# Kernel tuning notes

Measured on AMD Instinct MI355X. Metric: run time of the kernel, lower is better.

Reference implementation:

```python
import jax, jax.numpy as jnp
import numpy as np
from functools import partial

B, S, T = 32, 64, 64
VS, VT = 32000, 32000
E, H = 256, 512            # embed_dim, encoder hidden per direction
DH = 2 * H                 # decoder hidden (= encoder_hidden_dim)
A = 128                    # attention_dim


def _p(key, shape, scale=0.05):
    return scale * jax.random.normal(key, shape, dtype=jnp.float32)


def setup_inputs() -> dict:
    key = jax.random.key(0)
    ks = jax.random.split(key, 32)
    inp = {
        'src': jax.random.randint(ks[0], (B, S), 0, VS),
        'tgt_input': jax.random.randint(ks[1], (B, T), 0, VT),
        # encoder
        'enc_emb': _p(ks[2], (VS, E)),
        'enc_Wih_f': _p(ks[3], (4 * H, E)), 'enc_Whh_f': _p(ks[4], (4 * H, H)),
        'enc_bih_f': _p(ks[5], (4 * H,)),  'enc_bhh_f': _p(ks[6], (4 * H,)),
        'enc_Wih_b': _p(ks[7], (4 * H, E)), 'enc_Whh_b': _p(ks[8], (4 * H, H)),
        'enc_bih_b': _p(ks[9], (4 * H,)),  'enc_bhh_b': _p(ks[10], (4 * H,)),
        # decoder
        'dec_emb': _p(ks[11], (VT, E)),
        'Wd': _p(ks[12], (A, DH)), 'bd': _p(ks[13], (A,)),
        'We': _p(ks[14], (A, DH)), 'be': _p(ks[15], (A,)),
        'v_att': _p(ks[16], (A,)), 'bv': _p(ks[17], ()),
        'dec_Wih': _p(ks[18], (4 * DH, E + DH)), 'dec_Whh': _p(ks[19], (4 * DH, DH)),
        'dec_bih': _p(ks[20], (4 * DH,)), 'dec_bhh': _p(ks[21], (4 * DH,)),
        'Wo': _p(ks[22], (VT, DH + DH)), 'bo': _p(ks[23], (VT,)),
    }
    return inp


def _lstm_cell(x, h, c, Wih, Whh, b):
    g = x @ Wih.T + h @ Whh.T + b
    i, f, gg, o = jnp.split(g, 4, axis=-1)  # PyTorch gate order: i,f,g,o
    i, f, o = jax.nn.sigmoid(i), jax.nn.sigmoid(f), jax.nn.sigmoid(o)
    c_new = f * c + i * jnp.tanh(gg)
    h_new = o * jnp.tanh(c_new)
    return h_new, c_new


def _lstm_scan(xs, Wih, Whh, b, reverse):
    # xs: [S,B,E] -> outputs [S,B,H] aligned with input positions, final (h,c)
    h0 = jnp.zeros((xs.shape[1], Whh.shape[1]), xs.dtype)
    def step(carry, x):
        h, c = carry
        h, c = _lstm_cell(x, h, c, Wih, Whh, b)
        return (h, c), h
    (hT, cT), hs = jax.lax.scan(step, (h0, h0), xs, reverse=reverse)
    return hs, hT, cT


def _forward(src, tgt_input, enc_emb,
             enc_Wih_f, enc_Whh_f, enc_bih_f, enc_bhh_f,
             enc_Wih_b, enc_Whh_b, enc_bih_b, enc_bhh_b,
             dec_emb, Wd, bd, We, be, v_att, bv,
             dec_Wih, dec_Whh, dec_bih, dec_bhh, Wo, bo):
    # ---- Encoder: bidirectional single-layer LSTM ----
    emb = enc_emb[src]                              # [B,S,E]
    xs = emb.transpose(1, 0, 2)                     # [S,B,E]
    hs_f, hT_f, cT_f = _lstm_scan(xs, enc_Wih_f, enc_Whh_f, enc_bih_f + enc_bhh_f, False)
    hs_b, hT_b, cT_b = _lstm_scan(xs, enc_Wih_b, enc_Whh_b, enc_bih_b + enc_bhh_b, True)
    enc_out = jnp.concatenate([hs_f, hs_b], axis=-1).transpose(1, 0, 2)  # [B,S,2H]
    h = jnp.concatenate([hT_f, hT_b], axis=-1)      # [B,DH]
    c = jnp.concatenate([cT_f, cT_b], axis=-1)

    # ---- Decoder with Bahdanau attention (full teacher forcing) ----
    enc_proj = enc_out @ We.T + be                  # [B,S,A] precomputed
    dec_b = dec_bih + dec_bhh
    tgt_emb = dec_emb[tgt_input].transpose(1, 0, 2)  # [T,B,E]

    def dec_step(carry, emb_t):
        h, c = carry
        dproj = h @ Wd.T + bd                       # [B,A]
        energy = jnp.tanh(dproj[:, None, :] + enc_proj)  # [B,S,A]
        scores = energy @ v_att + bv                # [B,S]
        w = jax.nn.softmax(scores, axis=1)
        ctx = jnp.einsum('bs,bsh->bh', w, enc_out)  # [B,DH]
        x = jnp.concatenate([emb_t, ctx], axis=-1)  # [B,E+DH]
        h_new, c_new = _lstm_cell(x, h, c, dec_Wih, dec_Whh, dec_b)
        logits = jnp.concatenate([h_new, ctx], axis=-1) @ Wo.T + bo  # [B,VT]
        return (h_new, c_new), logits

    _, logits = jax.lax.scan(dec_step, (h, c), tgt_emb)  # [T,B,VT]
    return logits.transpose(1, 0, 2)                     # [B,T,VT]


def reference(src, tgt_input, enc_emb,
              enc_Wih_f, enc_Whh_f, enc_bih_f, enc_bhh_f,
              enc_Wih_b, enc_Whh_b, enc_bih_b, enc_bhh_b,
              dec_emb, Wd, bd, We, be, v_att, bv,
              dec_Wih, dec_Whh, dec_bih, dec_bhh, Wo, bo):
    return _forward(src, tgt_input, enc_emb,
                    enc_Wih_f, enc_Whh_f, enc_bih_f, enc_bhh_f,
                    enc_Wih_b, enc_Whh_b, enc_bih_b, enc_bhh_b,
                    dec_emb, Wd, bd, We, be, v_att, bv,
                    dec_Wih, dec_Whh, dec_bih, dec_bhh, Wo, bo)
```

## Files before the change

kernel.cpp:

```cpp
#include <hip/hip_runtime.h>


using u16 = unsigned short;
using u32 = unsigned int;
using u64 = unsigned long long;
using f32x4 = __attribute__((ext_vector_type(4))) float;
using s16x8 = __attribute__((ext_vector_type(8))) short;
using u16x4 = __attribute__((ext_vector_type(4))) unsigned short;

__device__ __forceinline__ float sigm_(float x) { return 1.0f / (1.0f + expf(-x)); }
__device__ __forceinline__ float tanh_(float x) {
    float e = __expf(fminf(2.0f * x, 30.0f));
    return (e - 1.0f) / (e + 1.0f);
}

__device__ __forceinline__ u16 f2bf(float x) {
    u32 u = __float_as_uint(x);
    u += 0x7fffu + ((u >> 16) & 1u);
    return (u16)(u >> 16);
}
__device__ __forceinline__ u32 pk2(float a, float b) {
    return (u32)f2bf(a) | ((u32)f2bf(b) << 16);
}
__device__ __forceinline__ float bf2f(u16 v) {
    return __uint_as_float((u32)v << 16);
}

__device__ __forceinline__ void ast32(u32* p, u32 v) {
    __hip_atomic_store(p, v, __ATOMIC_RELAXED, __HIP_MEMORY_SCOPE_AGENT);
}

#define MFMA __builtin_amdgcn_mfma_f32_16x16x32_bf16

#define GLL(g, l) __builtin_amdgcn_global_load_lds( \
    (__attribute__((address_space(1))) void*)(g),   \
    (__attribute__((address_space(3))) void*)(l), 16, 0, 0)

__device__ __forceinline__ void poll8(const int* go8) {
    if (threadIdx.x < 8) {
        const int* p = go8 + threadIdx.x * 16;
        while (__hip_atomic_load(p, __ATOMIC_RELAXED, __HIP_MEMORY_SCOPE_AGENT) == 0)
            __builtin_amdgcn_s_sleep(1);
    }
    __syncthreads();
    asm volatile("" ::: "memory");
}
__device__ __forceinline__ void arrive8(int* cnt8, int* go8, int line, int perline) {
    asm volatile("s_waitcnt vmcnt(0) lgkmcnt(0)" ::: "memory");
    __syncthreads();
    if (threadIdx.x == 0) {
        int old = __hip_atomic_fetch_add(cnt8 + line * 16, 1, __ATOMIC_RELAXED,
                                         __HIP_MEMORY_SCOPE_AGENT);
        if (old == perline - 1)
            __hip_atomic_store(go8 + line * 16, 1, __ATOMIC_RELAXED, __HIP_MEMORY_SCOPE_AGENT);
    }
}

__global__ __launch_bounds__(256) void k_zero(float* __restrict__ p, int n) {
    int i = blockIdx.x * 256 + threadIdx.x;
    if (i < n) p[i] = 0.0f;
}

__global__ __launch_bounds__(256) void k_cast_bf16(const float* __restrict__ in,
                                                   u16* __restrict__ outp, int n8) {
    int idx = blockIdx.x * 256 + threadIdx.x;
    if (idx >= n8) return;
    const f32x4* p = (const f32x4*)in + (size_t)idx * 2;
    f32x4 a = p[0], c = p[1];
    u32* o = (u32*)(outp + (size_t)idx * 8);
    o[0] = pk2(a.x, a.y); o[1] = pk2(a.z, a.w);
    o[2] = pk2(c.x, c.y); o[3] = pk2(c.z, c.w);
}

__global__ __launch_bounds__(256) void k_embed_bf(const int* __restrict__ tok,
                                                  const float* __restrict__ emb,
                                                  u16* __restrict__ outp) {
    int idx = blockIdx.x * 256 + threadIdx.x;
    int r = idx >> 6, e4 = idx & 63;
    int outer = r >> 5, b = r & 31;
    int tk = tok[b * 64 + outer];
    f32x4 v = ((const f32x4*)emb)[(size_t)tk * 64 + e4];
    u32* o = (u32*)(outp + (size_t)r * 256 + (e4 << 2));
    o[0] = pk2(v.x, v.y); o[1] = pk2(v.z, v.w);
}

__global__ __launch_bounds__(256) void k_prep_perm(
    const float* __restrict__ src, u16* __restrict__ dst,
    int J, int K4, int srcStride, int srcOff, int total)
{
    int idx = blockIdx.x * 256 + threadIdx.x;
    if (idx >= total) return;
    int n = idx / K4, kq = (idx - n * K4) << 2;
    int orig = (n & 3) * J + (n >> 2);
    f32x4 v = *(const f32x4*)(src + (size_t)orig * srcStride + srcOff + kq);
    u32* o = (u32*)(dst + (size_t)n * (K4 << 2) + kq);
    o[0] = pk2(v.x, v.y); o[1] = pk2(v.z, v.w);
}

__global__ __launch_bounds__(256) void k_prep_ws(
    const float* __restrict__ W, u16* __restrict__ dst)
{
    int idx = blockIdx.x * 256 + threadIdx.x;
    int n = idx >> 8, kp = idx & 255, k0 = kp << 1;
    int orig = (n & 3) * 512 + (n >> 2);
    const float* s = W + (size_t)orig * 512 + k0;
    int g = n >> 5, r = n & 31;
    int byteoff = (k0 << 1) ^ ((r & 7) << 4);
    *(u32*)((char*)dst + (size_t)g * 32768 + r * 1024 + byteoff) = pk2(s[0], s[1]);
}

__global__ __launch_bounds__(256) void k_prep_w2s(
    const float* __restrict__ Whh, const float* __restrict__ Wih, u16* __restrict__ dst)
{
    int idx = blockIdx.x * 256 + threadIdx.x;
    int n = idx >> 10, kp = idx & 1023, k0 = kp << 1;
    int orig = (n & 3) * 1024 + (n >> 2);
    const float* s = (k0 < 1024) ? (Whh + (size_t)orig * 1024 + k0)
                                 : (Wih + (size_t)orig * 1280 + 256 + (k0 - 1024));
    int g = n >> 5, r = n & 31;
    int byteoff = (k0 << 1) ^ ((r & 7) << 4);
    *(u32*)((char*)dst + (size_t)g * 131072 + r * 4096 + byteoff) = pk2(s[0], s[1]);
}

__global__ __launch_bounds__(256) void k_gemm_bf(
    const u16* __restrict__ A, const u16* __restrict__ B, int K,
    const float* __restrict__ b1, const float* __restrict__ b2, int biasJ,
    float* __restrict__ C, int ldc, int nM, int nN, int remapOut, int swz)
{
    __shared__ __align__(16) u16 As[128 * 32];
    __shared__ __align__(16) u16 Bs[128 * 32];
    int w = blockIdx.x;
    if (swz) { int cpx = (nM * nN) >> 3; w = (w & 7) * cpx + (w >> 3); }
    int bm = (w % nM) * 128, bn = (w / nM) * 128;
    int tid = threadIdx.x, wave = tid >> 6, lane = tid & 63;
    int wm = wave & 1, wn = wave >> 1;
    f32x4 acc[4][4] = {};

    int rA = wave * 32 + (lane >> 2);
    int cb2 = (lane & 3) * 16;
    const char* gA = (const char*)A + ((size_t)(bm + rA) * K) * 2 + cb2;
    const char* gB = (const char*)B + ((size_t)(bn + rA) * K) * 2 + cb2;
    size_t rowskip = (size_t)16 * K * 2;
    char* lA = (char*)As + wave * 2048;
    char* lB = (char*)Bs + wave * 2048;
    const u16* rdA = As + (wm * 64 + (lane & 15)) * 32 + (lane >> 4) * 8;
    const u16* rdB = Bs + (wn * 64 + (lane & 15)) * 32 + (lane >> 4) * 8;

    for (int k0 = 0; k0 < K; k0 += 32) {
        size_t kb = (size_t)k0 * 2;
        GLL(gA + kb, lA); GLL(gA + kb + rowskip, lA + 1024);
        GLL(gB + kb, lB); GLL(gB + kb + rowskip, lB + 1024);
        __syncthreads();
        s16x8 af[4], bfv[4];
#pragma unroll
        for (int m2 = 0; m2 < 4; ++m2) af[m2] = *(const s16x8*)(rdA + m2 * 512);
#pragma unroll
        for (int n2 = 0; n2 < 4; ++n2) bfv[n2] = *(const s16x8*)(rdB + n2 * 512);
#pragma unroll
        for (int m2 = 0; m2 < 4; ++m2)
#pragma unroll
            for (int n2 = 0; n2 < 4; ++n2)
                acc[m2][n2] = MFMA(af[m2], bfv[n2], acc[m2][n2], 0, 0, 0);
        __syncthreads();
    }

    int rbase = bm + wm * 64 + ((lane >> 4) << 2);
    int cbase = bn + wn * 64 + (lane & 15);
#pragma unroll
    for (int n2 = 0; n2 < 4; ++n2) {
        int col = cbase + n2 * 16;
        int bcol = biasJ ? ((col & 3) * biasJ + (col >> 2)) : col;
        float bias = (b1 ? b1[bcol] : 0.0f) + (b2 ? b2[bcol] : 0.0f);
#pragma unroll
        for (int m2 = 0; m2 < 4; ++m2) {
            f32x4 v = acc[m2][n2];
#pragma unroll
            for (int jj = 0; jj < 4; ++jj) {
                int row = rbase + m2 * 16 + jj;
                int orow = remapOut ? ((row & 31) * 64 + (row >> 5)) : row;
                C[(size_t)orow * ldc + col] = v[jj] + bias;
            }
        }
    }
}

__global__ __launch_bounds__(256, 1) void k_enc_persist(
    const u16* __restrict__ Wsf, const u16* __restrict__ Wsb,
    const float* __restrict__ Gfp, const float* __restrict__ Gbp,
    u16* __restrict__ henc,
    float* __restrict__ cfb,
    u16* __restrict__ encbf,
    int* __restrict__ cnt8, int* __restrict__ go8)
{
    __shared__ __align__(16) char smem[50176];
    int tid = threadIdx.x, lane = tid & 63, q = tid >> 6;
    int dir = blockIdx.x >> 6, g = blockIdx.x & 63;
    const char* wsrc = (const char*)(dir ? Wsb : Wsf) + (size_t)g * 32768;
#pragma unroll
    for (int it = 0; it < 8; ++it)
        GLL(wsrc + it * 4096 + tid * 16, smem + it * 4096 + tid * 16);
    __syncthreads();

    float* sacc = (float*)(smem + 32768);
    u16* hst = (u16*)(smem + 49664);
    const float* Gp = dir ? Gbp : Gfp;
    float* cB = cfb + dir * 16384;
    int lr = lane & 15, lk = (lane >> 4) << 3;
    int bb = tid & 31, jl = tid >> 5;
    int n0 = g * 32, j = g * 8 + jl;

    for (int s = 0; s < 64; ++s) {
        if (s) poll8(go8 + s * 128);
        int t = dir ? (63 - s) : s;
        f32x4 p4 = *(const f32x4*)(Gp + ((size_t)(t * 32 + bb)) * 2048 + n0 + (jl << 2));
        const u16* hA = henc + (size_t)s * 32768 + dir * 16384;
        s16x8 afr[8];
#pragma unroll
        for (int it = 0; it < 4; ++it) {
            int ke = q * 128 + it * 32 + lk;
            afr[2 * it]     = *(const s16x8*)(hA + lr * 512 + ke);
            afr[2 * it + 1] = *(const s16x8*)(hA + (lr + 16) * 512 + ke);
        }
        f32x4 acc00 = {}, acc01 = {}, acc10 = {}, acc11 = {};
#pragma unroll
        for (int it = 0; it < 4; ++it) {
            int ke = q * 128 + it * 32 + lk;
            int kb = ke << 1;
            s16x8 b0 = *(const s16x8*)(smem + lr * 1024 + (kb ^ ((lr & 7) << 4)));
            int r1 = lr + 16;
            s16x8 b1 = *(const s16x8*)(smem + r1 * 1024 + (kb ^ ((r1 & 7) << 4)));
            acc00 = MFMA(afr[2 * it], b0, acc00, 0, 0, 0);
            acc01 = MFMA(afr[2 * it], b1, acc01, 0, 0, 0);
            acc10 = MFMA(afr[2 * it + 1], b0, acc10, 0, 0, 0);
            acc11 = MFMA(afr[2 * it + 1], b1, acc11, 0, 0, 0);
        }
        int rw = (lane >> 4) << 2;
#pragma unroll
        for (int rr = 0; rr < 4; ++rr) {
            sacc[q * 1056 + (rw + rr) * 33 + lr]        = acc00[rr];
            sacc[q * 1056 + (rw + rr) * 33 + 16 + lr]   = acc01[rr];
            sacc[q * 1056 + (16 + rw + rr) * 33 + lr]      = acc10[rr];
            sacc[q * 1056 + (16 + rw + rr) * 33 + 16 + lr] = acc11[rr];
        }
        __syncthreads();
        {
            int c4 = jl << 2;
            float gi = 0, gf = 0, gg = 0, go2 = 0;
#pragma unroll
            for (int q2 = 0; q2 < 4; ++q2) {
                const float* sp = sacc + q2 * 1056 + bb * 33 + c4;
                gi += sp[0]; gf += sp[1]; gg += sp[2]; go2 += sp[3];
            }
            gi += p4.x; gf += p4.y; gg += p4.z; go2 += p4.w;
            float* cp = cB + bb * 512 + j;
            float cn = sigm_(gf) * cp[0] + sigm_(gi) * tanhf(gg);
            cp[0] = cn;
            float h = sigm_(go2) * tanhf(cn);
            u16 h16 = f2bf(h);
            encbf[((size_t)(bb * 64 + t)) * 1024 + dir * 512 + j] = h16;
            hst[bb * 8 + jl] = h16;
        }
        __syncthreads();
        if (tid < 128) {
            int bb2 = tid >> 2, p2 = tid & 3;
            u32 wv = (u32)hst[bb2 * 8 + 2 * p2] | ((u32)hst[bb2 * 8 + 2 * p2 + 1] << 16);
            ast32((u32*)(henc + (size_t)(s + 1) * 32768 + dir * 16384) + bb2 * 256 + g * 4 + p2, wv);
        }
        arrive8(cnt8 + (s + 1) * 128, go8 + (s + 1) * 128, blockIdx.x & 7, 16);
    }
}

__global__ __launch_bounds__(256) void k_dec_init(
    const u16* __restrict__ henc, const float* __restrict__ cfb,
    u16* __restrict__ hcarr, float* __restrict__ cd)
{
    int idx = blockIdx.x * 256 + threadIdx.x;
    int b = idx >> 10, j = idx & 1023;
    int dir = (j >> 9), jj = j & 511;
    hcarr[b * 2048 + j] = henc[(size_t)64 * 32768 + dir * 16384 + b * 512 + jj];
    cd[b * 1024 + j] = cfb[dir * 16384 + b * 512 + jj];
}

__global__ __launch_bounds__(256, 1) void k_dec_persist(
    const u16* __restrict__ W2s, const u16* __restrict__ encbf,
    const float* __restrict__ Prep,
    const u16* __restrict__ Wd_bf, const float* __restrict__ bd,
    const float* __restrict__ eproj, const float* __restrict__ v_att,
    const float* __restrict__ bv,
    u16* __restrict__ hcarr, float* __restrict__ cd, u16* __restrict__ Abf,
    int* __restrict__ hCnt8, int* __restrict__ goH8,
    int* __restrict__ ctxCnt8, int* __restrict__ goCtx8)
{
    __shared__ __align__(16) char smem[148480];
    int blk = blockIdx.x, tid = threadIdx.x, lane = tid & 63, q = tid >> 6;
    bool isgate = blk < 128;
    {
        const char* src = isgate ? ((const char*)W2s + (size_t)blk * 131072)
                                 : ((const char*)encbf + (size_t)(blk - 128) * 131072);
#pragma unroll
        for (int it = 0; it < 32; ++it)
            GLL(src + it * 4096 + tid * 16, smem + it * 4096 + tid * 16);
    }
    __syncthreads();

    float* sacc = (float*)(smem + 131072);
    u16* hst    = (u16*)(smem + 147968);
    float* hsh  = (float*)(smem + 131072);
    float* red  = (float*)(smem + 135168);
    float* dp   = (float*)(smem + 136192);
    float* sc   = (float*)(smem + 136704);

    int lr = lane & 15, lk = (lane >> 4) << 3;
    int bb = tid & 31, jl = tid >> 5;
    int n0 = blk * 32, j = blk * 8 + jl;
    int b = blk - 128;

    for (int t = 0; t < 64; ++t) {
        if (t) poll8(goH8 + t * 128);
        const u16* hcT = hcarr + (size_t)t * 65536;
        if (isgate) {
            f32x4 p4 = *(const f32x4*)(Prep + ((size_t)(t * 32 + bb)) * 4096 + n0 + (jl << 2));
            s16x8 afr[16];
#pragma unroll
            for (int it = 0; it < 8; ++it) {
                int ke = q * 256 + it * 32 + lk;
                afr[2 * it]     = *(const s16x8*)(hcT + lr * 2048 + ke);
                afr[2 * it + 1] = *(const s16x8*)(hcT + (lr + 16) * 2048 + ke);
            }
            f32x4 acc00 = {}, acc01 = {}, acc10 = {}, acc11 = {};
#pragma unroll
            for (int it = 0; it < 8; ++it) {
                int ke = q * 256 + it * 32 + lk;
                int kb = ke << 1;
                s16x8 b0 = *(const s16x8*)(smem + lr * 4096 + (kb ^ ((lr & 7) << 4)));
                int r1 = lr + 16;
                s16x8 b1 = *(const s16x8*)(smem + r1 * 4096 + (kb ^ ((r1 & 7) << 4)));
                acc00 = MFMA(afr[2 * it], b0, acc00, 0, 0, 0);
                acc01 = MFMA(afr[2 * it], b1, acc01, 0, 0, 0);
                acc10 = MFMA(afr[2 * it + 1], b0, acc10, 0, 0, 0);
                acc11 = MFMA(afr[2 * it + 1], b1, acc11, 0, 0, 0);
            }
            poll8(goCtx8 + t * 128);
#pragma unroll
            for (int it = 0; it < 8; ++it) {
                int ke = 1024 + q * 256 + it * 32 + lk;
                afr[2 * it]     = *(const s16x8*)(hcT + lr * 2048 + ke);
                afr[2 * it + 1] = *(const s16x8*)(hcT + (lr + 16) * 2048 + ke);
            }
#pragma unroll
            for (int it = 0; it < 8; ++it) {
                int ke = 1024 + q * 256 + it * 32 + lk;
                int kb = ke << 1;
                s16x8 b0 = *(const s16x8*)(smem + lr * 4096 + (kb ^ ((lr & 7) << 4)));
                int r1 = lr + 16;
                s16x8 b1 = *(const s16x8*)(smem + r1 * 4096 + (kb ^ ((r1 & 7) << 4)));
                acc00 = MFMA(afr[2 * it], b0, acc00, 0, 0, 0);
                acc01 = MFMA(afr[2 * it], b1, acc01, 0, 0, 0);
                acc10 = MFMA(afr[2 * it + 1], b0, acc10, 0, 0, 0);
                acc11 = MFMA(afr[2 * it + 1], b1, acc11, 0, 0, 0);
            }
            int rw = (lane >> 4) << 2;
#pragma unroll
            for (int rr = 0; rr < 4; ++rr) {
                sacc[q * 1056 + (rw + rr) * 33 + lr]        = acc00[rr];
                sacc[q * 1056 + (rw + rr) * 33 + 16 + lr]   = acc01[rr];
                sacc[q * 1056 + (16 + rw + rr) * 33 + lr]      = acc10[rr];
                sacc[q * 1056 + (16 + rw + rr) * 33 + 16 + lr] = acc11[rr];
            }
            __syncthreads();
            {
                int c4 = jl << 2;
                float gi = 0, gf = 0, gg = 0, go2 = 0;
#pragma unroll
                for (int q2 = 0; q2 < 4; ++q2) {
                    const float* sp = sacc + q2 * 1056 + bb * 33 + c4;
                    gi += sp[0]; gf += sp[1]; gg += sp[2]; go2 += sp[3];
                }
                gi += p4.x; gf += p4.y; gg += p4.z; go2 += p4.w;
                int ci = bb * 1024 + j;
                float cn = sigm_(gf) * cd[ci] + sigm_(gi) * tanhf(gg);
                cd[ci] = cn;
                float h = sigm_(go2) * tanhf(cn);
                u16 h16 = f2bf(h);
                Abf[((size_t)(t * 32 + bb)) * 2048 + j] = h16;
                hst[bb * 8 + jl] = h16;
            }
            __syncthreads();
            if (tid < 128) {
                int bb2 = tid >> 2, p2 = tid & 3;
                u32 wv = (u32)hst[bb2 * 8 + 2 * p2] | ((u32)hst[bb2 * 8 + 2 * p2 + 1] << 16);
                ast32((u32*)(hcarr + (size_t)(t + 1) * 65536) + bb2 * 1024 + blk * 4 + p2, wv);
            }
            arrive8(hCnt8 + (t + 1) * 128, goH8 + (t + 1) * 128, blk & 7, 16);
        } else {
            {
                u16x4 hv = *(const u16x4*)(hcT + b * 2048 + (tid << 2));
                hsh[(tid << 2) + 0] = bf2f(hv.x);
                hsh[(tid << 2) + 1] = bf2f(hv.y);
                hsh[(tid << 2) + 2] = bf2f(hv.z);
                hsh[(tid << 2) + 3] = bf2f(hv.w);
            }
            __syncthreads();
            {
                int a = tid & 127, half = tid >> 7;
                const u16* wr = Wd_bf + ((size_t)a << 10) + (half << 9);
                const float* hh = hsh + (half << 9);
                float s0 = 0, s1 = 0, s2 = 0, s3 = 0;
#pragma unroll 4
                for (int k = 0; k < 512; k += 32) {
                    s16x8 w0 = *(const s16x8*)(wr + k);
                    s16x8 w1 = *(const s16x8*)(wr + k + 8);
                    s16x8 w2 = *(const s16x8*)(wr + k + 16);
                    s16x8 w3 = *(const s16x8*)(wr + k + 24);
#pragma unroll
                    for (int e = 0; e < 8; ++e) {
                        s0 += bf2f((u16)w0[e]) * hh[k + e];
                        s1 += bf2f((u16)w1[e]) * hh[k + 8 + e];
                        s2 += bf2f((u16)w2[e]) * hh[k + 16 + e];
                        s3 += bf2f((u16)w3[e]) * hh[k + 24 + e];
                    }
                }
                red[tid] = (s0 + s1) + (s2 + s3);
            }
            __syncthreads();
            if (tid < 128) dp[tid] = red[tid] + red[tid + 128] + bd[tid];
            __syncthreads();
            {
                int si = tid >> 2, qq = tid & 3;
                const float* ep = eproj + ((size_t)(b * 64 + si)) * 128 + qq * 32;
                float s = 0.0f;
#pragma unroll 8
                for (int a2 = 0; a2 < 32; ++a2)
                    s += v_att[qq * 32 + a2] * tanh_(dp[qq * 32 + a2] + ep[a2]);
                red[tid] = s;
            }
            __syncthreads();
            if (tid < 64) {
                float x = red[tid * 4] + red[tid * 4 + 1] + red[tid * 4 + 2] + red[tid * 4 + 3] + bv[0];
                float mx = x;
#pragma unroll
                for (int off = 32; off; off >>= 1) mx = fmaxf(mx, __shfl_xor(mx, off));
                float e = __expf(x - mx), ss = e;
#pragma unroll
                for (int off = 32; off; off >>= 1) ss += __shfl_xor(ss, off);
                sc[tid] = e / ss;
            }
            __syncthreads();
            u32 cw0, cw1;
            {
                const u16* eL = (const u16*)smem;
                int c0i = tid << 2;
                float c0 = 0, c1 = 0, c2 = 0, c3 = 0;
                for (int s2 = 0; s2 < 64; ++s2) {
                    float wgt = sc[s2];
                    u16x4 rp = *(const u16x4*)(eL + s2 * 1024 + c0i);
                    c0 += wgt * bf2f(rp.x); c1 += wgt * bf2f(rp.y);
                    c2 += wgt * bf2f(rp.z); c3 += wgt * bf2f(rp.w);
                }
                cw0 = pk2(c0, c1); cw1 = pk2(c2, c3);
                u32* hw = (u32*)hcT + b * 1024 + 512 + (tid << 1);
                ast32(hw, cw0); ast32(hw + 1, cw1);
            }
            arrive8(ctxCnt8 + t * 128, goCtx8 + t * 128, blk & 7, 4);
            {
                u32* aw = (u32*)(Abf + ((size_t)(t * 32 + b)) * 2048 + 1024 + (tid << 2));
                aw[0] = cw0; aw[1] = cw1;
            }
        }
    }
}

extern "C" void kernel_launch(void* const* d_in, const int* in_sizes, int n_in,
                              void* d_out, int out_size, void* d_ws, size_t ws_size,
                              hipStream_t stream)
{
    (void)in_sizes; (void)n_in; (void)out_size; (void)ws_size;
    const int*   src     = (const int*)d_in[0];
    const int*   tgt     = (const int*)d_in[1];
    const float* enc_emb = (const float*)d_in[2];
    const float* eWih_f  = (const float*)d_in[3];
    const float* eWhh_f  = (const float*)d_in[4];
    const float* ebih_f  = (const float*)d_in[5];
    const float* ebhh_f  = (const float*)d_in[6];
    const float* eWih_b  = (const float*)d_in[7];
    const float* eWhh_b  = (const float*)d_in[8];
    const float* ebih_b  = (const float*)d_in[9];
    const float* ebhh_b  = (const float*)d_in[10];
    const float* dec_emb = (const float*)d_in[11];
    const float* Wd      = (const float*)d_in[12];
    const float* bd      = (const float*)d_in[13];
    const float* We      = (const float*)d_in[14];
    const float* be      = (const float*)d_in[15];
    const float* v_att   = (const float*)d_in[16];
    const float* bv      = (const float*)d_in[17];
    const float* dWih    = (const float*)d_in[18];
    const float* dWhh    = (const float*)d_in[19];
    const float* dbih    = (const float*)d_in[20];
    const float* dbhh    = (const float*)d_in[21];
    const float* Wo      = (const float*)d_in[22];
    const float* bo      = (const float*)d_in[23];
    float* out = (float*)d_out;

    char* wp = (char*)d_ws;
    auto alloc = [&](size_t nbytes) -> void* {
        void* p = (void*)wp;
        wp += (nbytes + 255) & ~(size_t)255;
        return p;
    };
    u16*   Xe_bf = (u16*)alloc(2048u * 256 * 2);
    u16*   Ed_bf = (u16*)alloc(2048u * 256 * 2);
    float* Gf_p  = (float*)alloc(2048u * 2048 * 4);
    float* Gb_p  = (float*)alloc(2048u * 2048 * 4);
    float* Pre_p = (float*)alloc(2048u * 4096 * 4);
    float* zr    = (float*)alloc(329728u);
    float* cfb   = zr;
    char*  sy    = (char*)zr + 131072;
    int*   cntE8 = (int*)(sy);
    int*   goE8  = (int*)(sy + 33280);
    int*   hCnt8 = (int*)(sy + 66560);
    int*   goH8  = (int*)(sy + 99840);
    int*   ctxC8 = (int*)(sy + 133120);
    int*   goX8  = (int*)(sy + 165888);
    u16*   henc  = (u16*)alloc(65u * 32768 * 2);
    u16*   hcarr = (u16*)alloc(65u * 65536 * 2);
    u16*   encbf = (u16*)alloc(2048u * 1024 * 2);
    float* eproj = (float*)alloc(2048u * 128 * 4);
    float* cd    = (float*)alloc(32768u * 4);
    u16*   Abf   = (u16*)alloc(2048u * 2048 * 2);
    u16*   Wbf   = (u16*)alloc(32000u * 2048 * 2);
    u16*   W2s   = (u16*)alloc(4096u * 2048 * 2);
    u16*   Wsf   = (u16*)alloc(2048u * 512 * 2);
    u16*   Wsb   = (u16*)alloc(2048u * 512 * 2);
    u16*   Wembf = (u16*)alloc(2048u * 256 * 2);
    u16*   Wembb = (u16*)alloc(2048u * 256 * 2);
    u16*   Wembd = (u16*)alloc(4096u * 256 * 2);
    u16*   We_bf = (u16*)alloc(128u * 1024 * 2);
    u16*   Wd_bf = (u16*)alloc(128u * 1024 * 2);

    k_zero<<<322, 256, 0, stream>>>(zr, 82432);
    k_zero<<<64, 256, 0, stream>>>((float*)henc, 16384);

    k_cast_bf16<<<32000, 256, 0, stream>>>(Wo, Wbf, 8192000);
    k_cast_bf16<<<64, 256, 0, stream>>>(We, We_bf, 16384);
    k_cast_bf16<<<64, 256, 0, stream>>>(Wd, Wd_bf, 16384);
    k_prep_perm<<<512, 256, 0, stream>>>(eWih_f, Wembf, 512, 64, 256, 0, 131072);
    k_prep_perm<<<512, 256, 0, stream>>>(eWih_b, Wembb, 512, 64, 256, 0, 131072);
    k_prep_perm<<<1024, 256, 0, stream>>>(dWih, Wembd, 1024, 64, 1280, 0, 262144);
    k_prep_ws<<<2048, 256, 0, stream>>>(eWhh_f, Wsf);
    k_prep_ws<<<2048, 256, 0, stream>>>(eWhh_b, Wsb);
    k_prep_w2s<<<16384, 256, 0, stream>>>(dWhh, dWih, W2s);

    k_embed_bf<<<512, 256, 0, stream>>>(src, enc_emb, Xe_bf);
    k_embed_bf<<<512, 256, 0, stream>>>(tgt, dec_emb, Ed_bf);

    k_gemm_bf<<<256, 256, 0, stream>>>(Xe_bf, Wembf, 256, ebih_f, ebhh_f, 512,
                                       Gf_p, 2048, 16, 16, 0, 1);
    k_gemm_bf<<<256, 256, 0, stream>>>(Xe_bf, Wembb, 256, ebih_b, ebhh_b, 512,
                                       Gb_p, 2048, 16, 16, 0, 1);
    k_gemm_bf<<<512, 256, 0, stream>>>(Ed_bf, Wembd, 256, dbih, dbhh, 1024,
                                       Pre_p, 4096, 16, 32, 0, 1);

    k_enc_persist<<<128, 256, 0, stream>>>(Wsf, Wsb, Gf_p, Gb_p, henc, cfb, encbf,
                                           cntE8, goE8);

    k_gemm_bf<<<16, 256, 0, stream>>>(encbf, We_bf, 1024, be, nullptr, 0,
                                      eproj, 128, 16, 1, 0, 1);
    k_dec_init<<<128, 256, 0, stream>>>(henc, cfb, hcarr, cd);

    k_dec_persist<<<160, 256, 0, stream>>>(W2s, encbf, Pre_p, Wd_bf, bd, eproj,
                                           v_att, bv, hcarr, cd, Abf,
                                           hCnt8, goH8, ctxC8, goX8);

    k_gemm_bf<<<4000, 256, 0, stream>>>(Abf, Wbf, 2048, bo, nullptr, 0,
                                        out, 32000, 16, 250, 1, 1);
}
```

Before: 2.015 ms.

## Overlap output projection GEMM with decoder recurrence inside persistent kernel

Adds 96 extra blocks to the persistent decoder kernel that compute the vocabulary projection (logits GEMM) for each group of four timesteps as soon as those rows of Abf are published, instead of running a separate GEMM after the recurrence. Abf writes now use atomic-style stores issued before the arrival flags so the consumer blocks see them. This hides the large output GEMM behind the latency-bound serial decoder loop. The risk is contention for compute and memory bandwidth with the recurrence blocks, and a leftover GEMM tail after the last step that uses only 96 blocks, fewer than the previous launch.

```diff
diff --git a/kernel.cpp b/kernel.cpp
--- a/kernel.cpp
+++ b/kernel.cpp
@@ -288,11 +288,73 @@
     const float* __restrict__ eproj, const float* __restrict__ v_att,
     const float* __restrict__ bv,
     u16* __restrict__ hcarr, float* __restrict__ cd, u16* __restrict__ Abf,
+    const u16* __restrict__ Wbf, const float* __restrict__ bo,
+    float* __restrict__ outp,
     int* __restrict__ hCnt8, int* __restrict__ goH8,
     int* __restrict__ ctxCnt8, int* __restrict__ goCtx8)
 {
     __shared__ __align__(16) char smem[148480];
     int blk = blockIdx.x, tid = threadIdx.x, lane = tid & 63, q = tid >> 6;
+
+    if (blk >= 160) {
+        int w = blk - 160;
+        u16* As = (u16*)smem;
+        u16* Bs = (u16*)(smem + 8192);
+        int wave = q, wm = wave & 1, wn = wave >> 1;
+        int rA = wave * 32 + (lane >> 2);
+        int cb2 = (lane & 3) * 16;
+        size_t rowskip = (size_t)16 * 2048 * 2;
+        char* lA = (char*)As + wave * 2048;
+        char* lB = (char*)Bs + wave * 2048;
+        const u16* rdA = As + (wm * 64 + (lane & 15)) * 32 + (lane >> 4) * 8;
+        const u16* rdB = Bs + (wn * 64 + (lane & 15)) * 32 + (lane >> 4) * 8;
+        for (int g = 0; g < 16; ++g) {
+            poll8(goH8 + (4 * g + 4) * 128);
+            int bm = g * 128;
+            const char* gA = (const char*)Abf + ((size_t)(bm + rA) * 2048) * 2 + cb2;
+            for (int nt = w; nt < 250; nt += 96) {
+                int bn = nt * 128;
+                const char* gB = (const char*)Wbf + ((size_t)(bn + rA) * 2048) * 2 + cb2;
+                f32x4 acc[4][4] = {};
+                for (int k0 = 0; k0 < 2048; k0 += 32) {
+                    size_t kb = (size_t)k0 * 2;
+                    GLL(gA + kb, lA); GLL(gA + kb + rowskip, lA + 1024);
+                    GLL(gB + kb, lB); GLL(gB + kb + rowskip, lB + 1024);
+                    __syncthreads();
+                    s16x8 af[4], bfv[4];
+#pragma unroll
+                    for (int m2 = 0; m2 < 4; ++m2) af[m2] = *(const s16x8*)(rdA + m2 * 512);
+#pragma unroll
+                    for (int n2 = 0; n2 < 4; ++n2) bfv[n2] = *(const s16x8*)(rdB + n2 * 512);
+#pragma unroll
+                    for (int m2 = 0; m2 < 4; ++m2)
+#pragma unroll
+                        for (int n2 = 0; n2 < 4; ++n2)
+                            acc[m2][n2] = MFMA(af[m2], bfv[n2], acc[m2][n2], 0, 0, 0);
+                    __syncthreads();
+                }
+                int rbase = bm + wm * 64 + ((lane >> 4) << 2);
+                int cbase = bn + wn * 64 + (lane & 15);
+#pragma unroll
+                for (int n2 = 0; n2 < 4; ++n2) {
+                    int col = cbase + n2 * 16;
+                    float bias = bo[col];
+#pragma unroll
+                    for (int m2 = 0; m2 < 4; ++m2) {
+                        f32x4 v = acc[m2][n2];
+#pragma unroll
+                        for (int jj = 0; jj < 4; ++jj) {
+                            int row = rbase + m2 * 16 + jj;
+                            int orow = (row & 31) * 64 + (row >> 5);
+                            outp[(size_t)orow * 32000 + col] = v[jj] + bias;
+                        }
+                    }
+                }
+            }
+        }
+        return;
+    }
+
     bool isgate = blk < 128;
     {
         const char* src = isgate ? ((const char*)W2s + (size_t)blk * 131072)
@@ -381,15 +443,14 @@
                 float cn = sigm_(gf) * cd[ci] + sigm_(gi) * tanhf(gg);
                 cd[ci] = cn;
                 float h = sigm_(go2) * tanhf(cn);
-                u16 h16 = f2bf(h);
-                Abf[((size_t)(t * 32 + bb)) * 2048 + j] = h16;
-                hst[bb * 8 + jl] = h16;
+                hst[bb * 8 + jl] = f2bf(h);
             }
             __syncthreads();
             if (tid < 128) {
                 int bb2 = tid >> 2, p2 = tid & 3;
                 u32 wv = (u32)hst[bb2 * 8 + 2 * p2] | ((u32)hst[bb2 * 8 + 2 * p2 + 1] << 16);
                 ast32((u32*)(hcarr + (size_t)(t + 1) * 65536) + bb2 * 1024 + blk * 4 + p2, wv);
+                ast32((u32*)Abf + (size_t)(t * 32 + bb2) * 1024 + blk * 4 + p2, wv);
             }
             arrive8(hCnt8 + (t + 1) * 128, goH8 + (t + 1) * 128, blk & 7, 16);
         } else {
@@ -446,7 +507,6 @@
                 sc[tid] = e / ss;
             }
             __syncthreads();
-            u32 cw0, cw1;
             {
                 const u16* eL = (const u16*)smem;
                 int c0i = tid << 2;
@@ -457,15 +517,13 @@
                     c0 += wgt * bf2f(rp.x); c1 += wgt * bf2f(rp.y);
                     c2 += wgt * bf2f(rp.z); c3 += wgt * bf2f(rp.w);
                 }
-                cw0 = pk2(c0, c1); cw1 = pk2(c2, c3);
+                u32 cw0 = pk2(c0, c1), cw1 = pk2(c2, c3);
                 u32* hw = (u32*)hcT + b * 1024 + 512 + (tid << 1);
                 ast32(hw, cw0); ast32(hw + 1, cw1);
+                u32* aw = (u32*)(Abf + ((size_t)(t * 32 + b)) * 2048 + 1024 + c0i);
+                ast32(aw, cw0); ast32(aw + 1, cw1);
             }
             arrive8(ctxCnt8 + t * 128, goCtx8 + t * 128, blk & 7, 4);
-            {
-                u32* aw = (u32*)(Abf + ((size_t)(t * 32 + b)) * 2048 + 1024 + (tid << 2));
-                aw[0] = cw0; aw[1] = cw1;
-            }
         }
     }
 }
@@ -567,10 +625,8 @@
                                       eproj, 128, 16, 1, 0, 1);
     k_dec_init<<<128, 256, 0, stream>>>(henc, cfb, hcarr, cd);
 
-    k_dec_persist<<<160, 256, 0, stream>>>(W2s, encbf, Pre_p, Wd_bf, bd, eproj,
+    k_dec_persist<<<256, 256, 0, stream>>>(W2s, encbf, Pre_p, Wd_bf, bd, eproj,
                                            v_att, bv, hcarr, cd, Abf,
+                                           Wbf, bo, out,
                                            hCnt8, goH8, ctxC8, goX8);
-
-    k_gemm_bf<<<4000, 256, 0, stream>>>(Abf, Wbf, 2048, bo, nullptr, 0,
-                                        out, 32000, 16, 250, 1, 1);
-}
+}
```

Result: slower. 2.280 ms (+13.1%).

## Overlap weight bf16 casts with encoder recurrence and use nontemporal output stores

Applied to the files above, without the earlier changes.

Moves the large Wo bf16 cast, the We/Wd casts and the decoder W2s weight repack into 128 extra blocks of the persistent encoder kernel. Those blocks do the conversion while the latency-bound encoder recurrence runs on the other 128 blocks, so the conversions no longer sit serially on the critical path. It also adds a nontemporal-store option to the GEMM and enables it for the final logits write. The risk is that the extra blocks compete with the encoder's spin-polling blocks for memory bandwidth and CUs, which could slow the recurrence.

```diff
diff --git a/kernel.cpp b/kernel.cpp
--- a/kernel.cpp
+++ b/kernel.cpp
@@ -59,17 +59,6 @@
 __global__ __launch_bounds__(256) void k_zero(float* __restrict__ p, int n) {
     int i = blockIdx.x * 256 + threadIdx.x;
     if (i < n) p[i] = 0.0f;
-}
-
-__global__ __launch_bounds__(256) void k_cast_bf16(const float* __restrict__ in,
-                                                   u16* __restrict__ outp, int n8) {
-    int idx = blockIdx.x * 256 + threadIdx.x;
-    if (idx >= n8) return;
-    const f32x4* p = (const f32x4*)in + (size_t)idx * 2;
-    f32x4 a = p[0], c = p[1];
-    u32* o = (u32*)(outp + (size_t)idx * 8);
-    o[0] = pk2(a.x, a.y); o[1] = pk2(a.z, a.w);
-    o[2] = pk2(c.x, c.y); o[3] = pk2(c.z, c.w);
 }
 
 __global__ __launch_bounds__(256) void k_embed_bf(const int* __restrict__ tok,
@@ -109,23 +98,10 @@
     *(u32*)((char*)dst + (size_t)g * 32768 + r * 1024 + byteoff) = pk2(s[0], s[1]);
 }
 
-__global__ __launch_bounds__(256) void k_prep_w2s(
-    const float* __restrict__ Whh, const float* __restrict__ Wih, u16* __restrict__ dst)
-{
-    int idx = blockIdx.x * 256 + threadIdx.x;
-    int n = idx >> 10, kp = idx & 1023, k0 = kp << 1;
-    int orig = (n & 3) * 1024 + (n >> 2);
-    const float* s = (k0 < 1024) ? (Whh + (size_t)orig * 1024 + k0)
-                                 : (Wih + (size_t)orig * 1280 + 256 + (k0 - 1024));
-    int g = n >> 5, r = n & 31;
-    int byteoff = (k0 << 1) ^ ((r & 7) << 4);
-    *(u32*)((char*)dst + (size_t)g * 131072 + r * 4096 + byteoff) = pk2(s[0], s[1]);
-}
-
 __global__ __launch_bounds__(256) void k_gemm_bf(
     const u16* __restrict__ A, const u16* __restrict__ B, int K,
     const float* __restrict__ b1, const float* __restrict__ b2, int biasJ,
-    float* __restrict__ C, int ldc, int nM, int nN, int remapOut, int swz)
+    float* __restrict__ C, int ldc, int nM, int nN, int remapOut, int swz, int ntStore)
 {
     __shared__ __align__(16) u16 As[128 * 32];
     __shared__ __align__(16) u16 Bs[128 * 32];
@@ -178,7 +154,10 @@
             for (int jj = 0; jj < 4; ++jj) {
                 int row = rbase + m2 * 16 + jj;
                 int orow = remapOut ? ((row & 31) * 64 + (row >> 5)) : row;
-                C[(size_t)orow * ldc + col] = v[jj] + bias;
+                float val = v[jj] + bias;
+                float* cp = C + (size_t)orow * ldc + col;
+                if (ntStore) __builtin_nontemporal_store(val, cp);
+                else *cp = val;
             }
         }
     }
@@ -190,10 +169,49 @@
     u16* __restrict__ henc,
     float* __restrict__ cfb,
     u16* __restrict__ encbf,
-    int* __restrict__ cnt8, int* __restrict__ go8)
+    int* __restrict__ cnt8, int* __restrict__ go8,
+    const float* __restrict__ Wo, u16* __restrict__ Wbf,
+    const float* __restrict__ We, u16* __restrict__ We_bf,
+    const float* __restrict__ Wd, u16* __restrict__ Wd_bf,
+    const float* __restrict__ dWhh, const float* __restrict__ dWih,
+    u16* __restrict__ W2s)
 {
     __shared__ __align__(16) char smem[50176];
     int tid = threadIdx.x, lane = tid & 63, q = tid >> 6;
+
+    if (blockIdx.x >= 128) {
+        int gt = (blockIdx.x - 128) * 256 + tid;
+        for (int i = gt; i < 8192000; i += 32768) {
+            const f32x4* p = (const f32x4*)Wo + (size_t)i * 2;
+            f32x4 a = p[0], c = p[1];
+            u32* o = (u32*)(Wbf + (size_t)i * 8);
+            o[0] = pk2(a.x, a.y); o[1] = pk2(a.z, a.w);
+            o[2] = pk2(c.x, c.y); o[3] = pk2(c.z, c.w);
+        }
+        if (gt < 16384) {
+            const f32x4* p = (const f32x4*)We + (size_t)gt * 2;
+            f32x4 a = p[0], c = p[1];
+            u32* o = (u32*)(We_bf + (size_t)gt * 8);
+            o[0] = pk2(a.x, a.y); o[1] = pk2(a.z, a.w);
+            o[2] = pk2(c.x, c.y); o[3] = pk2(c.z, c.w);
+            const f32x4* p2 = (const f32x4*)Wd + (size_t)gt * 2;
+            f32x4 a2 = p2[0], c2 = p2[1];
+            u32* o2 = (u32*)(Wd_bf + (size_t)gt * 8);
+            o2[0] = pk2(a2.x, a2.y); o2[1] = pk2(a2.z, a2.w);
+            o2[2] = pk2(c2.x, c2.y); o2[3] = pk2(c2.z, c2.w);
+        }
+        for (int i = gt; i < 4194304; i += 32768) {
+            int n = i >> 10, kp = i & 1023, k0 = kp << 1;
+            int orig = (n & 3) * 1024 + (n >> 2);
+            const float* s = (k0 < 1024) ? (dWhh + (size_t)orig * 1024 + k0)
+                                         : (dWih + (size_t)orig * 1280 + 256 + (k0 - 1024));
+            int g2 = n >> 5, r = n & 31;
+            int byteoff = (k0 << 1) ^ ((r & 7) << 4);
+            *(u32*)((char*)W2s + (size_t)g2 * 131072 + r * 4096 + byteoff) = pk2(s[0], s[1]);
+        }
+        return;
+    }
+
     int dir = blockIdx.x >> 6, g = blockIdx.x & 63;
     const char* wsrc = (const char*)(dir ? Wsb : Wsf) + (size_t)g * 32768;
 #pragma unroll
@@ -540,31 +558,29 @@
     k_zero<<<322, 256, 0, stream>>>(zr, 82432);
     k_zero<<<64, 256, 0, stream>>>((float*)henc, 16384);
 
-    k_cast_bf16<<<32000, 256, 0, stream>>>(Wo, Wbf, 8192000);
-    k_cast_bf16<<<64, 256, 0, stream>>>(We, We_bf, 16384);
-    k_cast_bf16<<<64, 256, 0, stream>>>(Wd, Wd_bf, 16384);
     k_prep_perm<<<512, 256, 0, stream>>>(eWih_f, Wembf, 512, 64, 256, 0, 131072);
     k_prep_perm<<<512, 256, 0, stream>>>(eWih_b, Wembb, 512, 64, 256, 0, 131072);
     k_prep_perm<<<1024, 256, 0, stream>>>(dWih, Wembd, 1024, 64, 1280, 0, 262144);
     k_prep_ws<<<2048, 256, 0, stream>>>(eWhh_f, Wsf);
     k_prep_ws<<<2048, 256, 0, stream>>>(eWhh_b, Wsb);
-    k_prep_w2s<<<16384, 256, 0, stream>>>(dWhh, dWih, W2s);
 
     k_embed_bf<<<512, 256, 0, stream>>>(src, enc_emb, Xe_bf);
     k_embed_bf<<<512, 256, 0, stream>>>(tgt, dec_emb, Ed_bf);
 
     k_gemm_bf<<<256, 256, 0, stream>>>(Xe_bf, Wembf, 256, ebih_f, ebhh_f, 512,
-                                       Gf_p, 2048, 16, 16, 0, 1);
+                                       Gf_p, 2048, 16, 16, 0, 1, 0);
     k_gemm_bf<<<256, 256, 0, stream>>>(Xe_bf, Wembb, 256, ebih_b, ebhh_b, 512,
-                                       Gb_p, 2048, 16, 16, 0, 1);
+                                       Gb_p, 2048, 16, 16, 0, 1, 0);
     k_gemm_bf<<<512, 256, 0, stream>>>(Ed_bf, Wembd, 256, dbih, dbhh, 1024,
-                                       Pre_p, 4096, 16, 32, 0, 1);
-
-    k_enc_persist<<<128, 256, 0, stream>>>(Wsf, Wsb, Gf_p, Gb_p, henc, cfb, encbf,
-                                           cntE8, goE8);
+                                       Pre_p, 4096, 16, 32, 0, 1, 0);
+
+    k_enc_persist<<<256, 256, 0, stream>>>(Wsf, Wsb, Gf_p, Gb_p, henc, cfb, encbf,
+                                           cntE8, goE8,
+                                           Wo, Wbf, We, We_bf, Wd, Wd_bf,
+                                           dWhh, dWih, W2s);
 
     k_gemm_bf<<<16, 256, 0, stream>>>(encbf, We_bf, 1024, be, nullptr, 0,
-                                      eproj, 128, 16, 1, 0, 1);
+                                      eproj, 128, 16, 1, 0, 1, 0);
     k_dec_init<<<128, 256, 0, stream>>>(henc, cfb, hcarr, cd);
 
     k_dec_persist<<<160, 256, 0, stream>>>(W2s, encbf, Pre_p, Wd_bf, bd, eproj,
@@ -572,5 +588,5 @@
                                            hCnt8, goH8, ctxC8, goX8);
 
     k_gemm_bf<<<4000, 256, 0, stream>>>(Abf, Wbf, 2048, bo, nullptr, 0,
-                                        out, 32000, 16, 250, 1, 1);
-}
+                                        out, 32000, 16, 250, 1, 1, 1);
+}
```

Result: faster. 1.953 ms, median of 2 (-3.1%).
